# Kernel tuning notes

Hardware: AMD Instinct MI355X
Metric: run time of the kernel (lower is better)

Reference implementation:

```python
import jax, jax.numpy as jnp
import numpy as np


def viterbi_decode(emissions, start_trans, trans, end_trans):
    """Batched Viterbi decode (pytorch-crf CRF.decode, full mask).
    emissions: [B,S,T] -> tags [B,S] int32."""
    score0 = start_trans[None, :] + emissions[:, 0]  # [B,T]

    def step(score, em_t):
        nxt = score[:, :, None] + trans[None, :, :]       # [B,T_prev,T_next]
        idx = jnp.argmax(nxt, axis=1)                     # best prev tag per next tag
        best = jnp.max(nxt, axis=1) + em_t                # [B,T]
        return best, idx

    score, hist = jax.lax.scan(step, score0, jnp.swapaxes(emissions[:, 1:], 0, 1))
    last = jnp.argmax(score + end_trans[None, :], axis=1)  # [B]

    def back(tag, h):
        prev = jnp.take_along_axis(h, tag[:, None], axis=1)[:, 0]
        return prev, prev

    _, prevs = jax.lax.scan(back, last, hist, reverse=True)  # [S-1,B]
    return jnp.concatenate([jnp.swapaxes(prevs, 0, 1), last[:, None]], axis=1)


def setup_inputs() -> dict:
    key = jax.random.key(0)
    ks = jax.random.split(key, 10)
    B, S, D, T, L, R = 4, 256, 768, 9, 30, 12
    H = D + L  # 798
    s = lambda d: 1.0 / np.sqrt(d)
    return {
        "embed": jax.random.normal(ks[0], (B, S, D), jnp.float32),
        "linear_w": jax.random.normal(ks[1], (D, T), jnp.float32) * s(D),
        "linear_b": jnp.zeros((T,), jnp.float32),
        "start_trans": jax.random.normal(ks[2], (T,), jnp.float32) * 0.1,
        "trans": jax.random.normal(ks[3], (T, T), jnp.float32) * 0.1,
        "end_trans": jax.random.normal(ks[4], (T,), jnp.float32) * 0.1,
        "label_emb": jax.random.normal(ks[5], (T, L), jnp.float32).at[0].set(0.0),  # padding_idx=0
        "U_w": jax.random.normal(ks[6], (H, H), jnp.float32) * s(H),
        "U_b": jnp.zeros((H,), jnp.float32),
        "W_w": jax.random.normal(ks[7], (H, H), jnp.float32) * s(H),
        "W_b": jnp.zeros((H,), jnp.float32),
        "V_w": jax.random.normal(ks[8], (H, R), jnp.float32) * s(H),
        "none_idx": 0,  # rel2idx['None']
    }


def reference(embed, linear_w, linear_b, start_trans, trans, end_trans,
              label_emb, U_w, U_b, W_w, W_b, V_w, none_idx):
    # NER head (dropout is identity in eval mode)
    ner = embed @ linear_w + linear_b                     # [B,S,T]
    tags = viterbi_decode(ner, start_trans, trans, end_trans)  # [B,S]
    hx = jnp.concatenate([embed, label_emb[tags]], axis=-1)    # [B,S,H]

    # Fused biaffine relation scoring over all (i=target, j=source) pairs:
    # score[b,i,j,:] = V(tanh(U(hx[b,i]) + W(hx[b,j])))
    u = hx @ U_w + U_b                                    # [B,S,H]
    w = hx @ W_w + W_b                                    # [B,S,H]
    pair = jnp.tanh(u[:, :, None, :] + w[:, None, :, :])  # [B,S,S,H]
    scores = jnp.einsum('bijh,hr->bijr', pair, V_w)       # [B,S,S,R]

    # p_head[:, i, rel2idx['None']] = 100 for target i -> diagonal set
    S = embed.shape[1]
    ii = jnp.arange(S)
    scores = scores.at[:, ii, ii, none_idx].set(100.0)
    return tags, scores
```

## Files before the change

kernel.cpp:

```cpp
#include <hip/hip_runtime.h>


typedef unsigned short ushort_t;
typedef __attribute__((ext_vector_type(8))) short bf16x8;
typedef __attribute__((ext_vector_type(4))) float f32x4;
typedef __attribute__((ext_vector_type(2))) float f32x2;
typedef __attribute__((ext_vector_type(4))) int i32x4;
typedef unsigned long long u64;

#define C2F 2.8853900817779268f

#define WS_UW2   0u
#define WS_NER   3276800u
#define WS_VFRAG 3313664u
#define WS_LAB2  3339264u
#define WS_TAGS  3396864u
#define WS_CSUM  3400960u

__device__ __forceinline__ unsigned f2b(float f){
  unsigned u = __float_as_uint(f);
  return (u + 0x7FFFu + ((u>>16)&1u)) >> 16;
}
__device__ __forceinline__ unsigned pkbf16(float hi, float lo){
  return __builtin_amdgcn_perm(__float_as_uint(hi), __float_as_uint(lo), 0x07060302u);
}
__device__ __forceinline__ float lo16(int v){ return __uint_as_float(((unsigned)v)<<16); }
__device__ __forceinline__ float hi16g(int v){ return __uint_as_float((unsigned)v); }
__device__ __forceinline__ u64 fcompose(u64 F, u64 H){
  u64 R = 0;
  #pragma unroll
  for (int t=0;t<9;t++){
    unsigned h = (unsigned)(H >> (4*t)) & 15u;
    unsigned v = (unsigned)(F >> (4*h)) & 15u;
    R |= (u64)v << (4*t);
  }
  return R;
}

__global__ __launch_bounds__(256) void gemm_prep_kernel(
    const float* __restrict__ embed, const float* __restrict__ lw,
    const float* __restrict__ lb,    const float* __restrict__ lemb,
    const float* __restrict__ uw,    const float* __restrict__ ub,
    const float* __restrict__ ww,    const float* __restrict__ wb,
    const float* __restrict__ vw,    char* __restrict__ ws)
{
  __shared__ char smem[10496];
  int bx = blockIdx.x, tid = threadIdx.x;
  if (bx < 400) {
    ushort_t (*As)[40] = (ushort_t(*)[40])smem;
    ushort_t (*Bs)[42] = (ushort_t(*)[42])(smem + 5120);
    ushort_t* uw2 = (ushort_t*)(ws + WS_UW2);
    int bm = bx & 15, bn = bx >> 4;
    int M0 = bm*64, N0 = bn*64;
    int w = tid>>6, lane = tid&63;
    int wr = w>>1, wc = w&1;
    int m16 = lane&15, quad = lane>>4;
    int nl = tid>>2, k8 = (tid&3)<<3;
    int bnn = tid & 63, bw = tid >> 6;
    int gn = N0 + bnn;
    const float* bsrc = uw; int bcol = 0; bool bzero = true;
    if (gn < 798)                    { bsrc = uw; bcol = gn;     bzero = false; }
    else if (gn >= 800 && gn < 1598) { bsrc = ww; bcol = gn-800; bzero = false; }

    f32x4 acc[2][2];
    #pragma unroll
    for (int mi=0;mi<2;mi++)
      #pragma unroll
      for (int ni=0;ni<2;ni++) acc[mi][ni] = (f32x4){0.f,0.f,0.f,0.f};

    f32x4 a_lo, a_hi; float bvals[8];
    {
      const float* ap = &embed[(M0+nl)*768 + k8];
      a_lo = *(const f32x4*)ap; a_hi = *(const f32x4*)(ap+4);
      #pragma unroll
      for (int r=0;r<4;r++) {
        int kk = r*8 + bw*2;
        bvals[2*r]   = bzero ? 0.f : bsrc[(kk  )*798 + bcol];
        bvals[2*r+1] = bzero ? 0.f : bsrc[(kk+1)*798 + bcol];
      }
    }
    for (int k0=0; k0<768; k0+=32) {
      i32x4 av = (i32x4){ (int)pkbf16(a_lo.y,a_lo.x), (int)pkbf16(a_lo.w,a_lo.z),
                          (int)pkbf16(a_hi.y,a_hi.x), (int)pkbf16(a_hi.w,a_hi.z) };
      *(i32x4*)&As[nl][k8] = av;
      #pragma unroll
      for (int r=0;r<4;r++) {
        int kk = r*8 + bw*2;
        *(unsigned*)&Bs[bnn][kk] = pkbf16(bvals[2*r+1], bvals[2*r]);
      }
      __syncthreads();
      if (k0 + 32 < 768) {
        const float* ap = &embed[(M0+nl)*768 + k0 + 32 + k8];
        a_lo = *(const f32x4*)ap; a_hi = *(const f32x4*)(ap+4);
        #pragma unroll
        for (int r=0;r<4;r++) {
          int kk = r*8 + bw*2;
          bvals[2*r]   = bzero ? 0.f : bsrc[(k0+32+kk  )*798 + bcol];
          bvals[2*r+1] = bzero ? 0.f : bsrc[(k0+32+kk+1)*798 + bcol];
        }
      }
      bf16x8 a0 = *(const bf16x8*)&As[wr*32      + m16][quad*8];
      bf16x8 a1 = *(const bf16x8*)&As[wr*32 + 16 + m16][quad*8];
      bf16x8 b0 = *(const bf16x8*)&Bs[wc*32      + m16][quad*8];
      bf16x8 b1 = *(const bf16x8*)&Bs[wc*32 + 16 + m16][quad*8];
      acc[0][0] = __builtin_amdgcn_mfma_f32_16x16x32_bf16(a0,b0,acc[0][0],0,0,0);
      acc[0][1] = __builtin_amdgcn_mfma_f32_16x16x32_bf16(a0,b1,acc[0][1],0,0,0);
      acc[1][0] = __builtin_amdgcn_mfma_f32_16x16x32_bf16(a1,b0,acc[1][0],0,0,0);
      acc[1][1] = __builtin_amdgcn_mfma_f32_16x16x32_bf16(a1,b1,acc[1][1],0,0,0);
      __syncthreads();
    }
    #pragma unroll
    for (int mi=0;mi<2;mi++)
      #pragma unroll
      for (int ni=0;ni<2;ni++)
        #pragma unroll
        for (int reg=0;reg<4;reg++) {
          int gm = M0 + wr*32 + mi*16 + quad*4 + reg;
          int go = N0 + wc*32 + ni*16 + m16;
          float bias = 0.f;
          if (go < 798) bias = ub[go];
          else if (go >= 800 && go < 1598) bias = wb[go-800];
          float v = (acc[mi][ni][reg] + bias) * C2F;
          uw2[gm*1600 + go] = (ushort_t)f2b(__builtin_amdgcn_exp2f(v));
        }
  } else if (bx < 450) {
    ushort_t* vf = (ushort_t*)(ws + WS_VFRAG);
    int idx = (bx-400)*256 + tid;
    int jj = idx & 7, lane = (idx>>3) & 63, c = idx >> 9;
    int h = c*32 + ((lane>>4)<<3) + jj;
    int n = lane & 15;
    vf[idx] = (h < 798 && n < 12) ? (ushort_t)f2b(vw[h*12 + n]) : (ushort_t)0;
  } else if (bx < 706) {
    float* ner = (float*)(ws + WS_NER);
    int w = tid >> 6, lane = tid & 63;
    int row = (bx-450)*4 + w;
    float acc[9];
    #pragma unroll
    for (int i=0;i<9;i++) acc[i]=0.f;
    const float* erow = embed + row*768;
    for (int kk=0; kk<12; kk++) {
      int k = kk*64 + lane;
      float e = erow[k];
      #pragma unroll
      for (int i=0;i<9;i++) acc[i] = __builtin_fmaf(e, lw[k*9+i], acc[i]);
    }
    #pragma unroll
    for (int i=0;i<9;i++) {
      float v = acc[i];
      for (int off=32; off>0; off>>=1) v += __shfl_down(v, off);
      if (lane == 0) ner[row*9+i] = v + lb[i];
    }
  } else if (bx < 763) {
    float* lab2 = (float*)(ws + WS_LAB2);
    int idx = (bx-706)*256 + tid;
    if (idx < 14400) {
      int g = idx / 1600, n = idx - g*1600;
      const float* X = (n < 800) ? uw : ww;
      int nn = (n < 800) ? n : (n - 800);
      float v = 1.0f;
      if (nn < 798) {
        float s = 0.f;
        for (int l=0;l<30;l++)
          s = __builtin_fmaf(lemb[g*30+l], X[(768+l)*798 + nn], s);
        v = __builtin_amdgcn_exp2f(s * C2F);
      }
      lab2[idx] = v;
    }
  } else {
    float* csum = (float*)(ws + WS_CSUM);
    if (tid < 12) {
      float s = 0.f;
      for (int h=0;h<798;h++) s += vw[h*12 + tid];
      csum[tid] = s;
    }
  }
}

__global__ __launch_bounds__(256) void viterbi_kernel(
    const float* __restrict__ start_t, const float* __restrict__ trans,
    const float* __restrict__ end_t,
    char* __restrict__ ws, float* __restrict__ out_tags)
{
  __shared__ char smem[46848];
  float* scores = (float*)smem;
  u64* pk = (u64*)(smem + 36864);
  float* trl = (float*)(smem + 45056);
  int* lastArr = (int*)(smem + 45384);
  unsigned char* tagbuf = (unsigned char*)(smem + 45400);
  const float* ner = (const float*)(ws + WS_NER);
  int* tags = (int*)(ws + WS_TAGS);
  int tid = threadIdx.x;
  int w = tid>>6, lane = tid&63;
  int b = w;
  int tt = lane < 9 ? lane : 8;
  if (tid < 81) trl[tid] = trans[tid];

  float tcol[9];
  #pragma unroll
  for (int p=0;p<9;p++) tcol[p] = trans[p*9+tt];
  const float* nb = ner + (b*256)*9 + tt;
  float score = start_t[tt] + nb[0];
  if (lane < 9) scores[(b*256 + 0)*9 + tt] = score;

  float cur[15], nxt[15];
  #pragma unroll
  for (int j=0;j<15;j++) cur[j] = nb[(1+j)*9];
  #define RL(p) (__uint_as_float(__builtin_amdgcn_readlane(__float_as_uint(score), p)) + tcol[p])
  for (int ch=0; ch<17; ch++) {
    int sb = 1 + ch*15;
    if (ch < 16) {
      #pragma unroll
      for (int j=0;j<15;j++) nxt[j] = nb[(sb+15+j)*9];
    }
    #pragma unroll
    for (int j=0;j<15;j++) {
      float m0 = fmaxf(fmaxf(RL(0),RL(1)),RL(2));
      float m1 = fmaxf(fmaxf(RL(3),RL(4)),RL(5));
      float m2 = fmaxf(fmaxf(RL(6),RL(7)),RL(8));
      score = fmaxf(fmaxf(m0,m1),m2) + cur[j];
      if (lane < 9) scores[(b*256 + sb + j)*9 + tt] = score;
    }
    #pragma unroll
    for (int j=0;j<15;j++) cur[j] = nxt[j];
  }
  {
    float fin = score + end_t[tt];
    #define RLF(p) __uint_as_float(__builtin_amdgcn_readlane(__float_as_uint(fin), p))
    float bv = RLF(0); int ba = 0;
    #pragma unroll
    for (int p=1;p<9;p++) { float v = RLF(p); if (v > bv) { bv = v; ba = p; } }
    if (lane == 0) lastArr[b] = ba;
    #undef RLF
  }
  #undef RL
  __syncthreads();

  for (int idx = tid; idx < 1024; idx += 256) {
    int bb = idx >> 8, s = idx & 255;
    u64 f;
    if (s == 255) f = 0x876543210ULL;
    else {
      const float* srow = &scores[(bb*256 + s)*9];
      float sp[9];
      #pragma unroll
      for (int p=0;p<9;p++) sp[p] = srow[p];
      f = 0;
      #pragma unroll
      for (int t=0;t<9;t++) {
        float best = sp[0] + trl[t]; int arg = 0;
        #pragma unroll
        for (int p=1;p<9;p++) {
          float v = sp[p] + trl[p*9 + t];
          if (v > best) { best = v; arg = p; }
        }
        f |= (u64)arg << (4*t);
      }
    }
    pk[bb*256 + s] = f;
  }
  __syncthreads();

  if (tid < 64) {
    int cb = tid >> 4, c = tid & 15;
    u64 fs[16];
    #pragma unroll
    for (int j=0;j<16;j++) fs[j] = pk[cb*256 + c*16 + j];
    u64 G = fs[15];
    #pragma unroll
    for (int j=14;j>=0;j--) G = fcompose(fs[j], G);
    u64 F = G;
    #pragma unroll
    for (int d=1; d<16; d<<=1) {
      u64 H = __shfl(F, tid + d);
      if (c + d < 16) F = fcompose(F, H);
    }
    int last = lastArr[cb];
    u64 Hn = __shfl(F, (c==15) ? tid : tid+1);
    unsigned t_cur = (c==15) ? (unsigned)last
                             : (unsigned)((Hn >> (4*last)) & 15u);
    #pragma unroll
    for (int j=15;j>=0;j--) {
      t_cur = (unsigned)((fs[j] >> (4*t_cur)) & 15u);
      tagbuf[cb*256 + c*16 + j] = (unsigned char)t_cur;
    }
  }
  __syncthreads();

  for (int idx = tid; idx < 1024; idx += 256) {
    int tg = (int)tagbuf[idx];
    tags[idx] = tg;
    out_tags[idx] = (float)tg;
  }
}

__global__ __launch_bounds__(256) void fuse_kernel(char* __restrict__ ws)
{
  ushort_t* uw2      = (ushort_t*)(ws + WS_UW2);
  const float* lab2  = (const float*)(ws + WS_LAB2);
  const int* tags    = (const int*)(ws + WS_TAGS);
  int idx = blockIdx.x*256 + threadIdx.x;
  int row = idx / 200, c8 = idx - row*200, kc = c8*8;
  int tag = tags[row];
  ushort_t* p = uw2 + (size_t)row*1600 + kc;
  i32x4 uv = *(const i32x4*)p;
  const float* lp = lab2 + tag*1600 + kc;
  f32x4 l0 = *(const f32x4*)lp;
  f32x4 l1 = *(const f32x4*)(lp+4);
  i32x4 q = (i32x4){ (int)pkbf16(hi16g(uv.x)*l0.y, lo16(uv.x)*l0.x),
                     (int)pkbf16(hi16g(uv.y)*l0.w, lo16(uv.y)*l0.z),
                     (int)pkbf16(hi16g(uv.z)*l1.y, lo16(uv.z)*l1.x),
                     (int)pkbf16(hi16g(uv.w)*l1.w, lo16(uv.w)*l1.z) };
  *(i32x4*)p = q;
}

__device__ __forceinline__ unsigned rpair(int uvw, int wvw){
  f32x2 xu; xu.x = lo16(uvw); xu.y = hi16g(uvw);
  f32x2 xw; xw.x = lo16(wvw); xw.y = hi16g(wvw);
  f32x2 one2 = {1.0f, 1.0f};
  f32x2 p;
  asm("v_pk_fma_f32 %0, %1, %2, %3" : "=v"(p) : "v"(xu), "v"(xw), "v"(one2));
  unsigned pb = __builtin_amdgcn_perm(__float_as_uint(p.y), __float_as_uint(p.x), 0x07060302u);
  unsigned magic2 = 0x7EF37EF3u;
  unsigned y;
  asm("v_pk_sub_u16 %0, %1, %2" : "=v"(y) : "v"(magic2), "v"(pb));
  return y;
}

__global__ __launch_bounds__(512) void scorer_kernel(
    char* __restrict__ ws, const int* __restrict__ none_p,
    float* __restrict__ d_out)
{
  __shared__ ushort_t sw[16][804];
  const ushort_t* uw2 = (const ushort_t*)(ws + WS_UW2);
  const ushort_t* vf  = (const ushort_t*)(ws + WS_VFRAG);
  const float* csum   = (const float*)(ws + WS_CSUM);
  float* out_sc = d_out + 1024;
  int bx = blockIdx.x, tid = threadIdx.x;
  int b = bx >> 8, ti = (bx>>4)&15, tj = bx&15;
  int I0 = ti*16, J0 = tj*16, bS = b*256;

  for (int idx = tid; idx < 1600; idx += 512) {
    int row = idx / 100, c8 = idx - row*100, kc = c8*8;
    int grow = bS + J0 + row;
    *(i32x4*)&sw[row][kc] = *(const i32x4*)(uw2 + (size_t)grow*1600 + 800 + kc);
  }
  __syncthreads();

  int lane = tid & 63, w = tid >> 6;
  int m16 = lane & 15, quad = lane >> 4;
  int none = *none_p;

  f32x4 acc[2];
  acc[0] = (f32x4){0.f,0.f,0.f,0.f};
  acc[1] = (f32x4){0.f,0.f,0.f,0.f};

  const ushort_t* su0 = uw2 + (size_t)(bS + I0 + w*2    )*1600 + quad*8;
  const ushort_t* su1 = uw2 + (size_t)(bS + I0 + w*2 + 1)*1600 + quad*8;
  const ushort_t* vlane = vf + lane*8;
  i32x4 bfc = *(const i32x4*)vlane;
  for (int c=0; c<25; c++) {
    i32x4 bfn;
    if (c < 24) bfn = *(const i32x4*)(vlane + (c+1)*512);
    int koff = c*32 + quad*8;
    i32x4 wv = *(const i32x4*)&sw[m16][koff];
    i32x4 uv0 = *(const i32x4*)(su0 + c*32);
    i32x4 uv1 = *(const i32x4*)(su1 + c*32);
    bf16x8 bfrag = __builtin_bit_cast(bf16x8, bfc);
    {
      unsigned a0 = rpair(uv0.x, wv.x);
      unsigned a1 = rpair(uv0.y, wv.y);
      unsigned a2 = rpair(uv0.z, wv.z);
      unsigned a3 = rpair(uv0.w, wv.w);
      i32x4 avv = (i32x4){(int)a0,(int)a1,(int)a2,(int)a3};
      bf16x8 af = __builtin_bit_cast(bf16x8, avv);
      acc[0] = __builtin_amdgcn_mfma_f32_16x16x32_bf16(af, bfrag, acc[0], 0,0,0);
    }
    {
      unsigned a0 = rpair(uv1.x, wv.x);
      unsigned a1 = rpair(uv1.y, wv.y);
      unsigned a2 = rpair(uv1.z, wv.z);
      unsigned a3 = rpair(uv1.w, wv.w);
      i32x4 avv = (i32x4){(int)a0,(int)a1,(int)a2,(int)a3};
      bf16x8 af = __builtin_bit_cast(bf16x8, avv);
      acc[1] = __builtin_amdgcn_mfma_f32_16x16x32_bf16(af, bfrag, acc[1], 0,0,0);
    }
    bfc = bfn;
  }

  int r = m16;
  if (r < 12) {
    float cs = csum[r];
    #pragma unroll
    for (int it=0; it<2; it++) {
      int gi = I0 + w*2 + it;
      #pragma unroll
      for (int reg=0; reg<4; reg++) {
        int gj = J0 + quad*4 + reg;
        float v = __builtin_fmaf(-2.0f, acc[it][reg], cs);
        if (gi == gj && r == none) v = 100.0f;
        out_sc[(size_t)((bS + gi)*256 + gj)*12 + r] = v;
      }
    }
  }
}

extern "C" void kernel_launch(void* const* d_in, const int* in_sizes, int n_in,
                              void* d_out, int out_size, void* d_ws, size_t ws_size,
                              hipStream_t stream)
{
  const float* embed = (const float*)d_in[0];
  const float* lw    = (const float*)d_in[1];
  const float* lb    = (const float*)d_in[2];
  const float* st    = (const float*)d_in[3];
  const float* tr    = (const float*)d_in[4];
  const float* et    = (const float*)d_in[5];
  const float* lemb  = (const float*)d_in[6];
  const float* uw    = (const float*)d_in[7];
  const float* ub    = (const float*)d_in[8];
  const float* ww    = (const float*)d_in[9];
  const float* wb    = (const float*)d_in[10];
  const float* vw    = (const float*)d_in[11];
  const int* none_p  = (const int*)d_in[12];
  char* ws = (char*)d_ws;
  float* out = (float*)d_out;

  hipLaunchKernelGGL(gemm_prep_kernel, dim3(764), dim3(256), 0, stream,
                     embed, lw, lb, lemb, uw, ub, ww, wb, vw, ws);
  hipLaunchKernelGGL(viterbi_kernel, dim3(1), dim3(256), 0, stream,
                     st, tr, et, ws, out);
  hipLaunchKernelGGL(fuse_kernel, dim3(800), dim3(256), 0, stream, ws);
  hipLaunchKernelGGL(scorer_kernel, dim3(1024), dim3(512), 0, stream,
                     ws, none_p, out);
}
```

Measured before the change: 167.6 us.

## Move embed GEMM after Viterbi and fuse label-factor multiply into epilogue

The bf16 MFMA GEMM for U/W projections moves out of the prep kernel into a new kernel that runs after Viterbi decoding. Its epilogue multiplies the exp2 result by the tag-dependent label factor directly, so the separate fuse pass (a read-modify-write of the whole uw2 buffer) is removed. The prep kernel shrinks to the NER, V-fragment, label and column-sum work, and the column sum is now spread over 96 threads with shuffles. The trade-off is that the GEMM can no longer overlap with or precede Viterbi, so it now sits on the critical path after the single-block Viterbi kernel. It also rounds to bf16 once instead of twice.

```diff
diff --git a/kernel.cpp b/kernel.cpp
--- a/kernel.cpp
+++ b/kernel.cpp
@@ -37,103 +37,17 @@
   return R;
 }
 
-__global__ __launch_bounds__(256) void gemm_prep_kernel(
+__global__ __launch_bounds__(256) void prep_kernel(
     const float* __restrict__ embed, const float* __restrict__ lw,
     const float* __restrict__ lb,    const float* __restrict__ lemb,
-    const float* __restrict__ uw,    const float* __restrict__ ub,
-    const float* __restrict__ ww,    const float* __restrict__ wb,
+    const float* __restrict__ uw,    const float* __restrict__ ww,
     const float* __restrict__ vw,    char* __restrict__ ws)
 {
-  __shared__ char smem[10496];
   int bx = blockIdx.x, tid = threadIdx.x;
-  if (bx < 400) {
-    ushort_t (*As)[40] = (ushort_t(*)[40])smem;
-    ushort_t (*Bs)[42] = (ushort_t(*)[42])(smem + 5120);
-    ushort_t* uw2 = (ushort_t*)(ws + WS_UW2);
-    int bm = bx & 15, bn = bx >> 4;
-    int M0 = bm*64, N0 = bn*64;
-    int w = tid>>6, lane = tid&63;
-    int wr = w>>1, wc = w&1;
-    int m16 = lane&15, quad = lane>>4;
-    int nl = tid>>2, k8 = (tid&3)<<3;
-    int bnn = tid & 63, bw = tid >> 6;
-    int gn = N0 + bnn;
-    const float* bsrc = uw; int bcol = 0; bool bzero = true;
-    if (gn < 798)                    { bsrc = uw; bcol = gn;     bzero = false; }
-    else if (gn >= 800 && gn < 1598) { bsrc = ww; bcol = gn-800; bzero = false; }
-
-    f32x4 acc[2][2];
-    #pragma unroll
-    for (int mi=0;mi<2;mi++)
-      #pragma unroll
-      for (int ni=0;ni<2;ni++) acc[mi][ni] = (f32x4){0.f,0.f,0.f,0.f};
-
-    f32x4 a_lo, a_hi; float bvals[8];
-    {
-      const float* ap = &embed[(M0+nl)*768 + k8];
-      a_lo = *(const f32x4*)ap; a_hi = *(const f32x4*)(ap+4);
-      #pragma unroll
-      for (int r=0;r<4;r++) {
-        int kk = r*8 + bw*2;
-        bvals[2*r]   = bzero ? 0.f : bsrc[(kk  )*798 + bcol];
-        bvals[2*r+1] = bzero ? 0.f : bsrc[(kk+1)*798 + bcol];
-      }
-    }
-    for (int k0=0; k0<768; k0+=32) {
-      i32x4 av = (i32x4){ (int)pkbf16(a_lo.y,a_lo.x), (int)pkbf16(a_lo.w,a_lo.z),
-                          (int)pkbf16(a_hi.y,a_hi.x), (int)pkbf16(a_hi.w,a_hi.z) };
-      *(i32x4*)&As[nl][k8] = av;
-      #pragma unroll
-      for (int r=0;r<4;r++) {
-        int kk = r*8 + bw*2;
-        *(unsigned*)&Bs[bnn][kk] = pkbf16(bvals[2*r+1], bvals[2*r]);
-      }
-      __syncthreads();
-      if (k0 + 32 < 768) {
-        const float* ap = &embed[(M0+nl)*768 + k0 + 32 + k8];
-        a_lo = *(const f32x4*)ap; a_hi = *(const f32x4*)(ap+4);
-        #pragma unroll
-        for (int r=0;r<4;r++) {
-          int kk = r*8 + bw*2;
-          bvals[2*r]   = bzero ? 0.f : bsrc[(k0+32+kk  )*798 + bcol];
-          bvals[2*r+1] = bzero ? 0.f : bsrc[(k0+32+kk+1)*798 + bcol];
-        }
-      }
-      bf16x8 a0 = *(const bf16x8*)&As[wr*32      + m16][quad*8];
-      bf16x8 a1 = *(const bf16x8*)&As[wr*32 + 16 + m16][quad*8];
-      bf16x8 b0 = *(const bf16x8*)&Bs[wc*32      + m16][quad*8];
-      bf16x8 b1 = *(const bf16x8*)&Bs[wc*32 + 16 + m16][quad*8];
-      acc[0][0] = __builtin_amdgcn_mfma_f32_16x16x32_bf16(a0,b0,acc[0][0],0,0,0);
-      acc[0][1] = __builtin_amdgcn_mfma_f32_16x16x32_bf16(a0,b1,acc[0][1],0,0,0);
-      acc[1][0] = __builtin_amdgcn_mfma_f32_16x16x32_bf16(a1,b0,acc[1][0],0,0,0);
-      acc[1][1] = __builtin_amdgcn_mfma_f32_16x16x32_bf16(a1,b1,acc[1][1],0,0,0);
-      __syncthreads();
-    }
-    #pragma unroll
-    for (int mi=0;mi<2;mi++)
-      #pragma unroll
-      for (int ni=0;ni<2;ni++)
-        #pragma unroll
-        for (int reg=0;reg<4;reg++) {
-          int gm = M0 + wr*32 + mi*16 + quad*4 + reg;
-          int go = N0 + wc*32 + ni*16 + m16;
-          float bias = 0.f;
-          if (go < 798) bias = ub[go];
-          else if (go >= 800 && go < 1598) bias = wb[go-800];
-          float v = (acc[mi][ni][reg] + bias) * C2F;
-          uw2[gm*1600 + go] = (ushort_t)f2b(__builtin_amdgcn_exp2f(v));
-        }
-  } else if (bx < 450) {
-    ushort_t* vf = (ushort_t*)(ws + WS_VFRAG);
-    int idx = (bx-400)*256 + tid;
-    int jj = idx & 7, lane = (idx>>3) & 63, c = idx >> 9;
-    int h = c*32 + ((lane>>4)<<3) + jj;
-    int n = lane & 15;
-    vf[idx] = (h < 798 && n < 12) ? (ushort_t)f2b(vw[h*12 + n]) : (ushort_t)0;
-  } else if (bx < 706) {
+  if (bx < 256) {
     float* ner = (float*)(ws + WS_NER);
     int w = tid >> 6, lane = tid & 63;
-    int row = (bx-450)*4 + w;
+    int row = bx*4 + w;
     float acc[9];
     #pragma unroll
     for (int i=0;i<9;i++) acc[i]=0.f;
@@ -150,9 +64,16 @@
       for (int off=32; off>0; off>>=1) v += __shfl_down(v, off);
       if (lane == 0) ner[row*9+i] = v + lb[i];
     }
-  } else if (bx < 763) {
+  } else if (bx < 306) {
+    ushort_t* vf = (ushort_t*)(ws + WS_VFRAG);
+    int idx = (bx-256)*256 + tid;
+    int jj = idx & 7, lane = (idx>>3) & 63, c = idx >> 9;
+    int h = c*32 + ((lane>>4)<<3) + jj;
+    int n = lane & 15;
+    vf[idx] = (h < 798 && n < 12) ? (ushort_t)f2b(vw[h*12 + n]) : (ushort_t)0;
+  } else if (bx < 363) {
     float* lab2 = (float*)(ws + WS_LAB2);
-    int idx = (bx-706)*256 + tid;
+    int idx = (bx-306)*256 + tid;
     if (idx < 14400) {
       int g = idx / 1600, n = idx - g*1600;
       const float* X = (n < 800) ? uw : ww;
@@ -168,10 +89,14 @@
     }
   } else {
     float* csum = (float*)(ws + WS_CSUM);
-    if (tid < 12) {
+    if (tid < 96) {
+      int r = tid >> 3, sub = tid & 7;
       float s = 0.f;
-      for (int h=0;h<798;h++) s += vw[h*12 + tid];
-      csum[tid] = s;
+      for (int h = sub; h < 798; h += 8) s += vw[h*12 + r];
+      s += __shfl_down(s, 4, 8);
+      s += __shfl_down(s, 2, 8);
+      s += __shfl_down(s, 1, 8);
+      if (sub == 0) csum[r] = s;
     }
   }
 }
@@ -293,24 +218,96 @@
   }
 }
 
-__global__ __launch_bounds__(256) void fuse_kernel(char* __restrict__ ws)
+__global__ __launch_bounds__(256) void gemm_fused_kernel(
+    const float* __restrict__ embed,
+    const float* __restrict__ uw,    const float* __restrict__ ub,
+    const float* __restrict__ ww,    const float* __restrict__ wb,
+    char* __restrict__ ws)
 {
-  ushort_t* uw2      = (ushort_t*)(ws + WS_UW2);
-  const float* lab2  = (const float*)(ws + WS_LAB2);
-  const int* tags    = (const int*)(ws + WS_TAGS);
-  int idx = blockIdx.x*256 + threadIdx.x;
-  int row = idx / 200, c8 = idx - row*200, kc = c8*8;
-  int tag = tags[row];
-  ushort_t* p = uw2 + (size_t)row*1600 + kc;
-  i32x4 uv = *(const i32x4*)p;
-  const float* lp = lab2 + tag*1600 + kc;
-  f32x4 l0 = *(const f32x4*)lp;
-  f32x4 l1 = *(const f32x4*)(lp+4);
-  i32x4 q = (i32x4){ (int)pkbf16(hi16g(uv.x)*l0.y, lo16(uv.x)*l0.x),
-                     (int)pkbf16(hi16g(uv.y)*l0.w, lo16(uv.y)*l0.z),
-                     (int)pkbf16(hi16g(uv.z)*l1.y, lo16(uv.z)*l1.x),
-                     (int)pkbf16(hi16g(uv.w)*l1.w, lo16(uv.w)*l1.z) };
-  *(i32x4*)p = q;
+  __shared__ char smem[10496];
+  int bx = blockIdx.x, tid = threadIdx.x;
+  ushort_t (*As)[40] = (ushort_t(*)[40])smem;
+  ushort_t (*Bs)[42] = (ushort_t(*)[42])(smem + 5120);
+  ushort_t* uw2 = (ushort_t*)(ws + WS_UW2);
+  const float* lab2 = (const float*)(ws + WS_LAB2);
+  const int* tags   = (const int*)(ws + WS_TAGS);
+  int bm = bx & 15, bn = bx >> 4;
+  int M0 = bm*64, N0 = bn*64;
+  int w = tid>>6, lane = tid&63;
+  int wr = w>>1, wc = w&1;
+  int m16 = lane&15, quad = lane>>4;
+  int nl = tid>>2, k8 = (tid&3)<<3;
+  int bnn = tid & 63, bw = tid >> 6;
+  int gn = N0 + bnn;
+  const float* bsrc = uw; int bcol = 0; bool bzero = true;
+  if (gn < 798)                    { bsrc = uw; bcol = gn;     bzero = false; }
+  else if (gn >= 800 && gn < 1598) { bsrc = ww; bcol = gn-800; bzero = false; }
+
+  f32x4 acc[2][2];
+  #pragma unroll
+  for (int mi=0;mi<2;mi++)
+    #pragma unroll
+    for (int ni=0;ni<2;ni++) acc[mi][ni] = (f32x4){0.f,0.f,0.f,0.f};
+
+  f32x4 a_lo, a_hi; float bvals[8];
+  {
+    const float* ap = &embed[(M0+nl)*768 + k8];
+    a_lo = *(const f32x4*)ap; a_hi = *(const f32x4*)(ap+4);
+    #pragma unroll
+    for (int r=0;r<4;r++) {
+      int kk = r*8 + bw*2;
+      bvals[2*r]   = bzero ? 0.f : bsrc[(kk  )*798 + bcol];
+      bvals[2*r+1] = bzero ? 0.f : bsrc[(kk+1)*798 + bcol];
+    }
+  }
+  for (int k0=0; k0<768; k0+=32) {
+    i32x4 av = (i32x4){ (int)pkbf16(a_lo.y,a_lo.x), (int)pkbf16(a_lo.w,a_lo.z),
+                        (int)pkbf16(a_hi.y,a_hi.x), (int)pkbf16(a_hi.w,a_hi.z) };
+    *(i32x4*)&As[nl][k8] = av;
+    #pragma unroll
+    for (int r=0;r<4;r++) {
+      int kk = r*8 + bw*2;
+      *(unsigned*)&Bs[bnn][kk] = pkbf16(bvals[2*r+1], bvals[2*r]);
+    }
+    __syncthreads();
+    if (k0 + 32 < 768) {
+      const float* ap = &embed[(M0+nl)*768 + k0 + 32 + k8];
+      a_lo = *(const f32x4*)ap; a_hi = *(const f32x4*)(ap+4);
+      #pragma unroll
+      for (int r=0;r<4;r++) {
+        int kk = r*8 + bw*2;
+        bvals[2*r]   = bzero ? 0.f : bsrc[(k0+32+kk  )*798 + bcol];
+        bvals[2*r+1] = bzero ? 0.f : bsrc[(k0+32+kk+1)*798 + bcol];
+      }
+    }
+    bf16x8 a0 = *(const bf16x8*)&As[wr*32      + m16][quad*8];
+    bf16x8 a1 = *(const bf16x8*)&As[wr*32 + 16 + m16][quad*8];
+    bf16x8 b0 = *(const bf16x8*)&Bs[wc*32      + m16][quad*8];
+    bf16x8 b1 = *(const bf16x8*)&Bs[wc*32 + 16 + m16][quad*8];
+    acc[0][0] = __builtin_amdgcn_mfma_f32_16x16x32_bf16(a0,b0,acc[0][0],0,0,0);
+    acc[0][1] = __builtin_amdgcn_mfma_f32_16x16x32_bf16(a0,b1,acc[0][1],0,0,0);
+    acc[1][0] = __builtin_amdgcn_mfma_f32_16x16x32_bf16(a1,b0,acc[1][0],0,0,0);
+    acc[1][1] = __builtin_amdgcn_mfma_f32_16x16x32_bf16(a1,b1,acc[1][1],0,0,0);
+    __syncthreads();
+  }
+  #pragma unroll
+  for (int mi=0;mi<2;mi++)
+    #pragma unroll
+    for (int reg=0;reg<4;reg++) {
+      int gm = M0 + wr*32 + mi*16 + quad*4 + reg;
+      int tg = tags[gm];
+      const float* lrow = lab2 + tg*1600;
+      #pragma unroll
+      for (int ni=0;ni<2;ni++) {
+        int go = N0 + wc*32 + ni*16 + m16;
+        float bias = 0.f;
+        if (go < 798) bias = ub[go];
+        else if (go >= 800 && go < 1598) bias = wb[go-800];
+        float v = (acc[mi][ni][reg] + bias) * C2F;
+        float e = __builtin_amdgcn_exp2f(v) * lrow[go];
+        uw2[gm*1600 + go] = (ushort_t)f2b(e);
+      }
+    }
 }
 
 __device__ __forceinline__ unsigned rpair(int uvw, int wvw){
@@ -424,11 +421,12 @@
   char* ws = (char*)d_ws;
   float* out = (float*)d_out;
 
-  hipLaunchKernelGGL(gemm_prep_kernel, dim3(764), dim3(256), 0, stream,
-                     embed, lw, lb, lemb, uw, ub, ww, wb, vw, ws);
+  hipLaunchKernelGGL(prep_kernel, dim3(364), dim3(256), 0, stream,
+                     embed, lw, lb, lemb, uw, ww, vw, ws);
   hipLaunchKernelGGL(viterbi_kernel, dim3(1), dim3(256), 0, stream,
                      st, tr, et, ws, out);
-  hipLaunchKernelGGL(fuse_kernel, dim3(800), dim3(256), 0, stream, ws);
+  hipLaunchKernelGGL(gemm_fused_kernel, dim3(400), dim3(256), 0, stream,
+                     embed, uw, ub, ww, wb, ws);
   hipLaunchKernelGGL(scorer_kernel, dim3(1024), dim3(512), 0, stream,
                      ws, none_p, out);
 }
```

Measured after the change: 186.4 us. 1.11x slower.

## Overlap Viterbi decode with GEMM by moving it into the prep kernel

Applied to the files above, without the earlier changes.

Splits the NER projection into its own small kernel launched first, then folds the single-block Viterbi decode into the main prep kernel as block 400. The serial decode now runs alongside the GEMM blocks instead of in a separate launch afterwards. The column-sum of V is also parallelised across 8 lanes per output with shuffle reductions. The cost is that the prep kernel now reserves 46.8KB of shared memory for every block, which may lower occupancy of the GEMM blocks.

```diff
diff --git a/kernel.cpp b/kernel.cpp
--- a/kernel.cpp
+++ b/kernel.cpp
@@ -37,15 +37,44 @@
   return R;
 }
 
-__global__ __launch_bounds__(256) void gemm_prep_kernel(
+__global__ __launch_bounds__(256) void ner_kernel(
     const float* __restrict__ embed, const float* __restrict__ lw,
-    const float* __restrict__ lb,    const float* __restrict__ lemb,
+    const float* __restrict__ lb,    char* __restrict__ ws)
+{
+  float* ner = (float*)(ws + WS_NER);
+  int bx = blockIdx.x, tid = threadIdx.x;
+  int w = tid >> 6, lane = tid & 63;
+  int row = bx*4 + w;
+  float acc[9];
+  #pragma unroll
+  for (int i=0;i<9;i++) acc[i]=0.f;
+  const float* erow = embed + row*768;
+  for (int kk=0; kk<12; kk++) {
+    int k = kk*64 + lane;
+    float e = erow[k];
+    #pragma unroll
+    for (int i=0;i<9;i++) acc[i] = __builtin_fmaf(e, lw[k*9+i], acc[i]);
+  }
+  #pragma unroll
+  for (int i=0;i<9;i++) {
+    float v = acc[i];
+    for (int off=32; off>0; off>>=1) v += __shfl_down(v, off);
+    if (lane == 0) ner[row*9+i] = v + lb[i];
+  }
+}
+
+__global__ __launch_bounds__(256) void main_kernel(
+    const float* __restrict__ embed, const float* __restrict__ lemb,
     const float* __restrict__ uw,    const float* __restrict__ ub,
     const float* __restrict__ ww,    const float* __restrict__ wb,
-    const float* __restrict__ vw,    char* __restrict__ ws)
+    const float* __restrict__ vw,
+    const float* __restrict__ start_t, const float* __restrict__ trans,
+    const float* __restrict__ end_t,
+    char* __restrict__ ws, float* __restrict__ out_tags)
 {
-  __shared__ char smem[10496];
+  __shared__ char smem[46848];
   int bx = blockIdx.x, tid = threadIdx.x;
+
   if (bx < 400) {
     ushort_t (*As)[40] = (ushort_t(*)[40])smem;
     ushort_t (*Bs)[42] = (ushort_t(*)[42])(smem + 5120);
@@ -123,36 +152,118 @@
           float v = (acc[mi][ni][reg] + bias) * C2F;
           uw2[gm*1600 + go] = (ushort_t)f2b(__builtin_amdgcn_exp2f(v));
         }
-  } else if (bx < 450) {
-    ushort_t* vf = (ushort_t*)(ws + WS_VFRAG);
-    int idx = (bx-400)*256 + tid;
-    int jj = idx & 7, lane = (idx>>3) & 63, c = idx >> 9;
-    int h = c*32 + ((lane>>4)<<3) + jj;
-    int n = lane & 15;
-    vf[idx] = (h < 798 && n < 12) ? (ushort_t)f2b(vw[h*12 + n]) : (ushort_t)0;
-  } else if (bx < 706) {
-    float* ner = (float*)(ws + WS_NER);
-    int w = tid >> 6, lane = tid & 63;
-    int row = (bx-450)*4 + w;
-    float acc[9];
-    #pragma unroll
-    for (int i=0;i<9;i++) acc[i]=0.f;
-    const float* erow = embed + row*768;
-    for (int kk=0; kk<12; kk++) {
-      int k = kk*64 + lane;
-      float e = erow[k];
-      #pragma unroll
-      for (int i=0;i<9;i++) acc[i] = __builtin_fmaf(e, lw[k*9+i], acc[i]);
-    }
-    #pragma unroll
-    for (int i=0;i<9;i++) {
-      float v = acc[i];
-      for (int off=32; off>0; off>>=1) v += __shfl_down(v, off);
-      if (lane == 0) ner[row*9+i] = v + lb[i];
-    }
-  } else if (bx < 763) {
+  } else if (bx == 400) {
+    float* scores = (float*)smem;
+    u64* pk = (u64*)(smem + 36864);
+    float* trl = (float*)(smem + 45056);
+    int* lastArr = (int*)(smem + 45384);
+    unsigned char* tagbuf = (unsigned char*)(smem + 45400);
+    const float* ner = (const float*)(ws + WS_NER);
+    int* tags = (int*)(ws + WS_TAGS);
+    int w = tid>>6, lane = tid&63;
+    int b = w;
+    int tt = lane < 9 ? lane : 8;
+    if (tid < 81) trl[tid] = trans[tid];
+
+    float tcol[9];
+    #pragma unroll
+    for (int p=0;p<9;p++) tcol[p] = trans[p*9+tt];
+    const float* nb = ner + (b*256)*9 + tt;
+    float score = start_t[tt] + nb[0];
+    if (lane < 9) scores[(b*256 + 0)*9 + tt] = score;
+
+    float cur[15], nxt[15];
+    #pragma unroll
+    for (int j=0;j<15;j++) cur[j] = nb[(1+j)*9];
+    #define RL(p) (__uint_as_float(__builtin_amdgcn_readlane(__float_as_uint(score), p)) + tcol[p])
+    for (int ch=0; ch<17; ch++) {
+      int sb = 1 + ch*15;
+      if (ch < 16) {
+        #pragma unroll
+        for (int j=0;j<15;j++) nxt[j] = nb[(sb+15+j)*9];
+      }
+      #pragma unroll
+      for (int j=0;j<15;j++) {
+        float m0 = fmaxf(fmaxf(RL(0),RL(1)),RL(2));
+        float m1 = fmaxf(fmaxf(RL(3),RL(4)),RL(5));
+        float m2 = fmaxf(fmaxf(RL(6),RL(7)),RL(8));
+        score = fmaxf(fmaxf(m0,m1),m2) + cur[j];
+        if (lane < 9) scores[(b*256 + sb + j)*9 + tt] = score;
+      }
+      #pragma unroll
+      for (int j=0;j<15;j++) cur[j] = nxt[j];
+    }
+    {
+      float fin = score + end_t[tt];
+      #define RLF(p) __uint_as_float(__builtin_amdgcn_readlane(__float_as_uint(fin), p))
+      float bv = RLF(0); int ba = 0;
+      #pragma unroll
+      for (int p=1;p<9;p++) { float v = RLF(p); if (v > bv) { bv = v; ba = p; } }
+      if (lane == 0) lastArr[b] = ba;
+      #undef RLF
+    }
+    #undef RL
+    __syncthreads();
+
+    for (int idx = tid; idx < 1024; idx += 256) {
+      int bb = idx >> 8, s = idx & 255;
+      u64 f;
+      if (s == 255) f = 0x876543210ULL;
+      else {
+        const float* srow = &scores[(bb*256 + s)*9];
+        float sp[9];
+        #pragma unroll
+        for (int p=0;p<9;p++) sp[p] = srow[p];
+        f = 0;
+        #pragma unroll
+        for (int t=0;t<9;t++) {
+          float best = sp[0] + trl[t]; int arg = 0;
+          #pragma unroll
+          for (int p=1;p<9;p++) {
+            float v = sp[p] + trl[p*9 + t];
+            if (v > best) { best = v; arg = p; }
+          }
+          f |= (u64)arg << (4*t);
+        }
+      }
+      pk[bb*256 + s] = f;
+    }
+    __syncthreads();
+
+    if (tid < 64) {
+      int cb = tid >> 4, c = tid & 15;
+      u64 fs[16];
+      #pragma unroll
+      for (int j=0;j<16;j++) fs[j] = pk[cb*256 + c*16 + j];
+      u64 G = fs[15];
+      #pragma unroll
+      for (int j=14;j>=0;j--) G = fcompose(fs[j], G);
+      u64 F = G;
+      #pragma unroll
+      for (int d=1; d<16; d<<=1) {
+        u64 H = __shfl(F, tid + d);
+        if (c + d < 16) F = fcompose(F, H);
+      }
+      int last = lastArr[cb];
+      u64 Hn = __shfl(F, (c==15) ? tid : tid+1);
+      unsigned t_cur = (c==15) ? (unsigned)last
+                               : (unsigned)((Hn >> (4*last)) & 15u);
+      #pragma unroll
+      for (int j=15;j>=0;j--) {
+        t_cur = (unsigned)((fs[j] >> (4*t_cur)) & 15u);
+        tagbuf[cb*256 + c*16 + j] = (unsigned char)t_cur;
+      }
+    }
+    __syncthreads();
+
+    for (int idx = tid; idx < 1024; idx += 256) {
+      int tg = (int)tagbuf[idx];
+      tags[idx] = tg;
+      out_tags[idx] = (float)tg;
+    }
+  } else if (bx < 458) {
     float* lab2 = (float*)(ws + WS_LAB2);
-    int idx = (bx-706)*256 + tid;
+    int idx = (bx-401)*256 + tid;
     if (idx < 14400) {
       int g = idx / 1600, n = idx - g*1600;
       const float* X = (n < 800) ? uw : ww;
@@ -166,130 +277,26 @@
       }
       lab2[idx] = v;
     }
+  } else if (bx < 508) {
+    ushort_t* vf = (ushort_t*)(ws + WS_VFRAG);
+    int idx = (bx-458)*256 + tid;
+    if (idx < 12800) {
+      int jj = idx & 7, lane = (idx>>3) & 63, c = idx >> 9;
+      int h = c*32 + ((lane>>4)<<3) + jj;
+      int n = lane & 15;
+      vf[idx] = (h < 798 && n < 12) ? (ushort_t)f2b(vw[h*12 + n]) : (ushort_t)0;
+    }
   } else {
     float* csum = (float*)(ws + WS_CSUM);
-    if (tid < 12) {
+    if (tid < 96) {
+      int r = tid >> 3, sub = tid & 7;
       float s = 0.f;
-      for (int h=0;h<798;h++) s += vw[h*12 + tid];
-      csum[tid] = s;
-    }
-  }
-}
-
-__global__ __launch_bounds__(256) void viterbi_kernel(
-    const float* __restrict__ start_t, const float* __restrict__ trans,
-    const float* __restrict__ end_t,
-    char* __restrict__ ws, float* __restrict__ out_tags)
-{
-  __shared__ char smem[46848];
-  float* scores = (float*)smem;
-  u64* pk = (u64*)(smem + 36864);
-  float* trl = (float*)(smem + 45056);
-  int* lastArr = (int*)(smem + 45384);
-  unsigned char* tagbuf = (unsigned char*)(smem + 45400);
-  const float* ner = (const float*)(ws + WS_NER);
-  int* tags = (int*)(ws + WS_TAGS);
-  int tid = threadIdx.x;
-  int w = tid>>6, lane = tid&63;
-  int b = w;
-  int tt = lane < 9 ? lane : 8;
-  if (tid < 81) trl[tid] = trans[tid];
-
-  float tcol[9];
-  #pragma unroll
-  for (int p=0;p<9;p++) tcol[p] = trans[p*9+tt];
-  const float* nb = ner + (b*256)*9 + tt;
-  float score = start_t[tt] + nb[0];
-  if (lane < 9) scores[(b*256 + 0)*9 + tt] = score;
-
-  float cur[15], nxt[15];
-  #pragma unroll
-  for (int j=0;j<15;j++) cur[j] = nb[(1+j)*9];
-  #define RL(p) (__uint_as_float(__builtin_amdgcn_readlane(__float_as_uint(score), p)) + tcol[p])
-  for (int ch=0; ch<17; ch++) {
-    int sb = 1 + ch*15;
-    if (ch < 16) {
-      #pragma unroll
-      for (int j=0;j<15;j++) nxt[j] = nb[(sb+15+j)*9];
-    }
-    #pragma unroll
-    for (int j=0;j<15;j++) {
-      float m0 = fmaxf(fmaxf(RL(0),RL(1)),RL(2));
-      float m1 = fmaxf(fmaxf(RL(3),RL(4)),RL(5));
-      float m2 = fmaxf(fmaxf(RL(6),RL(7)),RL(8));
-      score = fmaxf(fmaxf(m0,m1),m2) + cur[j];
-      if (lane < 9) scores[(b*256 + sb + j)*9 + tt] = score;
-    }
-    #pragma unroll
-    for (int j=0;j<15;j++) cur[j] = nxt[j];
-  }
-  {
-    float fin = score + end_t[tt];
-    #define RLF(p) __uint_as_float(__builtin_amdgcn_readlane(__float_as_uint(fin), p))
-    float bv = RLF(0); int ba = 0;
-    #pragma unroll
-    for (int p=1;p<9;p++) { float v = RLF(p); if (v > bv) { bv = v; ba = p; } }
-    if (lane == 0) lastArr[b] = ba;
-    #undef RLF
-  }
-  #undef RL
-  __syncthreads();
-
-  for (int idx = tid; idx < 1024; idx += 256) {
-    int bb = idx >> 8, s = idx & 255;
-    u64 f;
-    if (s == 255) f = 0x876543210ULL;
-    else {
-      const float* srow = &scores[(bb*256 + s)*9];
-      float sp[9];
-      #pragma unroll
-      for (int p=0;p<9;p++) sp[p] = srow[p];
-      f = 0;
-      #pragma unroll
-      for (int t=0;t<9;t++) {
-        float best = sp[0] + trl[t]; int arg = 0;
-        #pragma unroll
-        for (int p=1;p<9;p++) {
-          float v = sp[p] + trl[p*9 + t];
-          if (v > best) { best = v; arg = p; }
-        }
-        f |= (u64)arg << (4*t);
-      }
-    }
-    pk[bb*256 + s] = f;
-  }
-  __syncthreads();
-
-  if (tid < 64) {
-    int cb = tid >> 4, c = tid & 15;
-    u64 fs[16];
-    #pragma unroll
-    for (int j=0;j<16;j++) fs[j] = pk[cb*256 + c*16 + j];
-    u64 G = fs[15];
-    #pragma unroll
-    for (int j=14;j>=0;j--) G = fcompose(fs[j], G);
-    u64 F = G;
-    #pragma unroll
-    for (int d=1; d<16; d<<=1) {
-      u64 H = __shfl(F, tid + d);
-      if (c + d < 16) F = fcompose(F, H);
-    }
-    int last = lastArr[cb];
-    u64 Hn = __shfl(F, (c==15) ? tid : tid+1);
-    unsigned t_cur = (c==15) ? (unsigned)last
-                             : (unsigned)((Hn >> (4*last)) & 15u);
-    #pragma unroll
-    for (int j=15;j>=0;j--) {
-      t_cur = (unsigned)((fs[j] >> (4*t_cur)) & 15u);
-      tagbuf[cb*256 + c*16 + j] = (unsigned char)t_cur;
-    }
-  }
-  __syncthreads();
-
-  for (int idx = tid; idx < 1024; idx += 256) {
-    int tg = (int)tagbuf[idx];
-    tags[idx] = tg;
-    out_tags[idx] = (float)tg;
+      for (int h = sub; h < 798; h += 8) s += vw[h*12 + r];
+      s += __shfl_down(s, 4, 8);
+      s += __shfl_down(s, 2, 8);
+      s += __shfl_down(s, 1, 8);
+      if (sub == 0) csum[r] = s;
+    }
   }
 }
 
@@ -424,10 +431,10 @@
   char* ws = (char*)d_ws;
   float* out = (float*)d_out;
 
-  hipLaunchKernelGGL(gemm_prep_kernel, dim3(764), dim3(256), 0, stream,
-                     embed, lw, lb, lemb, uw, ub, ww, wb, vw, ws);
-  hipLaunchKernelGGL(viterbi_kernel, dim3(1), dim3(256), 0, stream,
-                     st, tr, et, ws, out);
+  hipLaunchKernelGGL(ner_kernel, dim3(256), dim3(256), 0, stream,
+                     embed, lw, lb, ws);
+  hipLaunchKernelGGL(main_kernel, dim3(509), dim3(256), 0, stream,
+                     embed, lemb, uw, ub, ww, wb, vw, st, tr, et, ws, out);
   hipLaunchKernelGGL(fuse_kernel, dim3(800), dim3(256), 0, stream, ws);
   hipLaunchKernelGGL(scorer_kernel, dim3(1024), dim3(512), 0, stream,
                      ws, none_p, out);
```

After: 147.7 us. 11.8% less time.
